# Kernel tuning notes

Measured on AMD Instinct MI355X. Metric: run time of the kernel, lower is better.

The kernel has to match this reference:

```python
import jax, jax.numpy as jnp
import numpy as np

MARGIN = 1.0  # from init_kwargs
B, H, W, P = 64, 512, 640, 100000


def setup_inputs() -> dict:
    key = jax.random.key(0)
    k0, k1, k2, k3, k4, k5 = jax.random.split(key, 6)
    return {
        "inp": jax.random.normal(k0, (B, 1, H, W), dtype=jnp.float32),
        "x_A": jax.random.randint(k1, (B, P), 0, W, dtype=jnp.int32),
        "y_A": jax.random.randint(k2, (B, P), 0, H, dtype=jnp.int32),
        "x_B": jax.random.randint(k3, (B, P), 0, W, dtype=jnp.int32),
        "y_B": jax.random.randint(k4, (B, P), 0, H, dtype=jnp.int32),
        "ordinal": jax.random.randint(k5, (B, P), 0, 3, dtype=jnp.int32),
    }


def reference(inp, x_A, y_A, x_B, y_B, ordinal):
    # inp: [B,1,H,W]; point coords: [B,P]; ordinal in {0,1,2} -> gt in {-1,0,1}
    depth = inp[:, 0]                                   # [B,H,W]
    bidx = jnp.arange(depth.shape[0])[:, None]          # [B,1]
    z_A = depth[bidx, y_A, x_A]                         # [B,P] gather
    z_B = depth[bidx, y_B, x_B]                         # [B,P] gather
    gt = (ordinal - 1).astype(depth.dtype)              # {-1,0,1}
    mask = jnp.abs(gt)
    zd = z_A - z_B
    m = jnp.asarray(MARGIN, depth.dtype)
    # ordered pairs: log(1+exp(-min(gt*zd, m))); equal pairs: max(zd^2, m^2)
    loss = mask * jnp.log(1.0 + jnp.exp(-jnp.minimum(gt * zd, m))) \
         + (1.0 - mask) * jnp.maximum(zd * zd, m * m)
    n_point_total = depth.shape[0] * x_A.shape[1]
    return jnp.sum(loss) / n_point_total
```

## Files before the change

### kernel.cpp

```cpp
#include <hip/hip_runtime.h>


constexpr int B = 64;
constexpr int H = 512;
constexpr int W = 640;
constexpr int P = 100000;
constexpr int N4B = P / 4;
constexpr int IPB = 512;
constexpr int CHUNKS = (N4B + IPB - 1) / IPB;
constexpr int NBLK = B * CHUNKS;
constexpr float INV_N = 1.0f / (float)(B * P);
constexpr float MARGIN = 1.0f;

typedef int vint4 __attribute__((ext_vector_type(4)));

__device__ __forceinline__ float loss_from(float za, float zb, int od) {
    float zd = za - zb;
    float gt = (float)(od - 1);
    float mask = fabsf(gt);
    float t = fminf(gt * zd, MARGIN);
    float l_rank = __logf(1.0f + __expf(-t));
    float l_eq = fmaxf(zd * zd, MARGIN * MARGIN);
    return mask * l_rank + (1.0f - mask) * l_eq;
}

__global__ __launch_bounds__(256) void rdc_kernel(
        const float* __restrict__ depth,
        const vint4* __restrict__ xA, const vint4* __restrict__ yA,
        const vint4* __restrict__ xB, const vint4* __restrict__ yB,
        const vint4* __restrict__ ord,
        float* __restrict__ partials) {
    __shared__ float zbuf[4][16][64];

    int j = blockIdx.x;
    int x = j & 7;
    int g = j >> 3;
    int b = ((g / CHUNKS) << 3) + x;
    int c = g % CHUNKS;
    int e0 = c * IPB + threadIdx.x;
    int e1 = e0 + 256;

    float s1 = (e1 < N4B) ? 1.0f : 0.0f;
    int i0 = b * N4B + e0;
    int i1 = b * N4B + (e1 < N4B ? e1 : e0);

    const float* d = depth + (size_t)b * (H * W);
    int lane = threadIdx.x & 63;
    int wid  = threadIdx.x >> 6;

    vint4 xa0 = __builtin_nontemporal_load(&xA[i0]);
    vint4 ya0 = __builtin_nontemporal_load(&yA[i0]);
    vint4 xb0 = __builtin_nontemporal_load(&xB[i0]);
    vint4 yb0 = __builtin_nontemporal_load(&yB[i0]);
    vint4 od0 = __builtin_nontemporal_load(&ord[i0]);
    vint4 xa1 = __builtin_nontemporal_load(&xA[i1]);
    vint4 ya1 = __builtin_nontemporal_load(&yA[i1]);
    vint4 xb1 = __builtin_nontemporal_load(&xB[i1]);
    vint4 yb1 = __builtin_nontemporal_load(&yB[i1]);
    vint4 od1 = __builtin_nontemporal_load(&ord[i1]);

    int off[16];
    off[0]  = ya0.x * W + xa0.x;  off[1]  = yb0.x * W + xb0.x;
    off[2]  = ya0.y * W + xa0.y;  off[3]  = yb0.y * W + xb0.y;
    off[4]  = ya0.z * W + xa0.z;  off[5]  = yb0.z * W + xb0.z;
    off[6]  = ya0.w * W + xa0.w;  off[7]  = yb0.w * W + xb0.w;
    off[8]  = ya1.x * W + xa1.x;  off[9]  = yb1.x * W + xb1.x;
    off[10] = ya1.y * W + xa1.y;  off[11] = yb1.y * W + xb1.y;
    off[12] = ya1.z * W + xa1.z;  off[13] = yb1.z * W + xb1.z;
    off[14] = ya1.w * W + xa1.w;  off[15] = yb1.w * W + xb1.w;

    #pragma unroll
    for (int k = 0; k < 16; ++k) {
        __builtin_amdgcn_global_load_lds(
            (const __attribute__((address_space(1))) void*)(d + off[k]),
            (__attribute__((address_space(3))) void*)&zbuf[wid][k][0],
            4, 0, 0);
    }
    __syncthreads();

    float z[16];
    #pragma unroll
    for (int k = 0; k < 16; ++k)
        z[k] = zbuf[wid][k][lane];

    float acc = 0.0f;
    acc += loss_from(z[0],  z[1],  od0.x);
    acc += loss_from(z[2],  z[3],  od0.y);
    acc += loss_from(z[4],  z[5],  od0.z);
    acc += loss_from(z[6],  z[7],  od0.w);
    float acc1 = 0.0f;
    acc1 += loss_from(z[8],  z[9],  od1.x);
    acc1 += loss_from(z[10], z[11], od1.y);
    acc1 += loss_from(z[12], z[13], od1.z);
    acc1 += loss_from(z[14], z[15], od1.w);
    acc += s1 * acc1;

    #pragma unroll
    for (int off2 = 32; off2 > 0; off2 >>= 1)
        acc += __shfl_down(acc, off2, 64);

    __shared__ float wsum[4];
    if (lane == 0) wsum[wid] = acc;
    __syncthreads();
    if (wid == 0 && lane == 0)
        partials[j] = wsum[0] + wsum[1] + wsum[2] + wsum[3];
}

__global__ __launch_bounds__(256) void rdc_finalize(
        const float* __restrict__ partials, float* __restrict__ out, int n) {
    float acc = 0.0f;
    for (int k = threadIdx.x; k < n; k += 256)
        acc += partials[k];
    #pragma unroll
    for (int off = 32; off > 0; off >>= 1)
        acc += __shfl_down(acc, off, 64);
    __shared__ float wsum[4];
    int lane = threadIdx.x & 63;
    int wid  = threadIdx.x >> 6;
    if (lane == 0) wsum[wid] = acc;
    __syncthreads();
    if (wid == 0 && lane == 0)
        out[0] = (wsum[0] + wsum[1] + wsum[2] + wsum[3]) * INV_N;
}

extern "C" void kernel_launch(void* const* d_in, const int* in_sizes, int n_in,
                              void* d_out, int out_size, void* d_ws, size_t ws_size,
                              hipStream_t stream) {
    const float* depth = (const float*)d_in[0];
    const vint4* xA = (const vint4*)d_in[1];
    const vint4* yA = (const vint4*)d_in[2];
    const vint4* xB = (const vint4*)d_in[3];
    const vint4* yB = (const vint4*)d_in[4];
    const vint4* ord = (const vint4*)d_in[5];
    float* out = (float*)d_out;

    float* partials = (float*)d_ws;
    rdc_kernel<<<NBLK, 256, 0, stream>>>(depth, xA, yA, xB, yB, ord, partials);
    rdc_finalize<<<1, 256, 0, stream>>>(partials, out, NBLK);
}
```

Baseline: 242.5 us.

## Replace random depth gathers with tiled LDS sweep over each image

Each block now owns one chunk of a batch's point pairs (8 chunks per image) and streams the whole depth image through double-buffered LDS tiles of 16K floats. Each thread keeps 56 flat pixel keys in registers and picks up values whenever a key falls in the current tile, so scattered global gathers become coalesced streaming reads. Ordinal values are packed into 2 bits to save registers. The cost is that every chunk re-reads the full image (8x per image, about 670MB in total) plus a 56-way compare loop over 20 tiles, with heavy register pressure.

```diff
diff --git a/kernel.cpp b/kernel.cpp
--- a/kernel.cpp
+++ b/kernel.cpp
@@ -5,10 +5,16 @@
 constexpr int H = 512;
 constexpr int W = 640;
 constexpr int P = 100000;
+constexpr int HWSZ = H * W;
 constexpr int N4B = P / 4;
-constexpr int IPB = 512;
-constexpr int CHUNKS = (N4B + IPB - 1) / IPB;
-constexpr int NBLK = B * CHUNKS;
+constexpr int NCHUNK = 8;
+constexpr int C4 = N4B / NCHUNK;
+constexpr int THREADS = 512;
+constexpr int SLOTS = 7;
+constexpr int NG = SLOTS * 8;
+constexpr int TE = 16384;
+constexpr int T = HWSZ / TE;
+constexpr int NBLK = B * NCHUNK;
 constexpr float INV_N = 1.0f / (float)(B * P);
 constexpr float MARGIN = 1.0f;
 
@@ -24,86 +30,110 @@
     return mask * l_rank + (1.0f - mask) * l_eq;
 }
 
-__global__ __launch_bounds__(256) void rdc_kernel(
+__device__ __forceinline__ void stage_tile(const float* __restrict__ src,
+                                           float* dst, int wid, int lane) {
+    #pragma unroll
+    for (int l = 0; l < 8; ++l) {
+        int cb = (wid * 8 + l) * 256;
+        __builtin_amdgcn_global_load_lds(
+            (const __attribute__((address_space(1))) void*)(src + cb + lane * 4),
+            (__attribute__((address_space(3))) void*)(dst + cb),
+            16, 0, 0);
+    }
+}
+
+__global__ __launch_bounds__(THREADS) void rdc_sweep(
         const float* __restrict__ depth,
         const vint4* __restrict__ xA, const vint4* __restrict__ yA,
         const vint4* __restrict__ xB, const vint4* __restrict__ yB,
         const vint4* __restrict__ ord,
         float* __restrict__ partials) {
-    __shared__ float zbuf[4][16][64];
+    __shared__ float tiles[2][TE];
+    __shared__ float wsum[8];
 
-    int j = blockIdx.x;
-    int x = j & 7;
-    int g = j >> 3;
-    int b = ((g / CHUNKS) << 3) + x;
-    int c = g % CHUNKS;
-    int e0 = c * IPB + threadIdx.x;
-    int e1 = e0 + 256;
+    const int j = blockIdx.x;
+    const int x = j & 7;
+    const int g = j >> 3;
+    const int chunk = g & 7;
+    const int b = ((g >> 3) << 3) + x;
 
-    float s1 = (e1 < N4B) ? 1.0f : 0.0f;
-    int i0 = b * N4B + e0;
-    int i1 = b * N4B + (e1 < N4B ? e1 : e0);
+    const int tid = threadIdx.x;
+    const int lane = tid & 63;
+    const int wid = tid >> 6;
 
-    const float* d = depth + (size_t)b * (H * W);
-    int lane = threadIdx.x & 63;
-    int wid  = threadIdx.x >> 6;
+    const float* dimg = depth + (size_t)b * HWSZ;
 
-    vint4 xa0 = __builtin_nontemporal_load(&xA[i0]);
-    vint4 ya0 = __builtin_nontemporal_load(&yA[i0]);
-    vint4 xb0 = __builtin_nontemporal_load(&xB[i0]);
-    vint4 yb0 = __builtin_nontemporal_load(&yB[i0]);
-    vint4 od0 = __builtin_nontemporal_load(&ord[i0]);
-    vint4 xa1 = __builtin_nontemporal_load(&xA[i1]);
-    vint4 ya1 = __builtin_nontemporal_load(&yA[i1]);
-    vint4 xb1 = __builtin_nontemporal_load(&xB[i1]);
-    vint4 yb1 = __builtin_nontemporal_load(&yB[i1]);
-    vint4 od1 = __builtin_nontemporal_load(&ord[i1]);
+    stage_tile(dimg, &tiles[0][0], wid, lane);
 
-    int off[16];
-    off[0]  = ya0.x * W + xa0.x;  off[1]  = yb0.x * W + xb0.x;
-    off[2]  = ya0.y * W + xa0.y;  off[3]  = yb0.y * W + xb0.y;
-    off[4]  = ya0.z * W + xa0.z;  off[5]  = yb0.z * W + xb0.z;
-    off[6]  = ya0.w * W + xa0.w;  off[7]  = yb0.w * W + xb0.w;
-    off[8]  = ya1.x * W + xa1.x;  off[9]  = yb1.x * W + xb1.x;
-    off[10] = ya1.y * W + xa1.y;  off[11] = yb1.y * W + xb1.y;
-    off[12] = ya1.z * W + xa1.z;  off[13] = yb1.z * W + xb1.z;
-    off[14] = ya1.w * W + xa1.w;  off[15] = yb1.w * W + xb1.w;
+    const int base4 = b * N4B + chunk * C4;
+    int key[NG];
+    int pack[SLOTS];
+    #pragma unroll
+    for (int i = 0; i < SLOTS; ++i) {
+        int c = i * THREADS + tid;
+        if (c > C4 - 1) c = C4 - 1;
+        int idx = base4 + c;
+        vint4 xa = __builtin_nontemporal_load(&xA[idx]);
+        vint4 ya = __builtin_nontemporal_load(&yA[idx]);
+        vint4 xb = __builtin_nontemporal_load(&xB[idx]);
+        vint4 yb = __builtin_nontemporal_load(&yB[idx]);
+        vint4 od = __builtin_nontemporal_load(&ord[idx]);
+        key[i*8+0] = ya.x * W + xa.x;  key[i*8+1] = yb.x * W + xb.x;
+        key[i*8+2] = ya.y * W + xa.y;  key[i*8+3] = yb.y * W + xb.y;
+        key[i*8+4] = ya.z * W + xa.z;  key[i*8+5] = yb.z * W + xb.z;
+        key[i*8+6] = ya.w * W + xa.w;  key[i*8+7] = yb.w * W + xb.w;
+        pack[i] = (od.x & 3) | ((od.y & 3) << 2) | ((od.z & 3) << 4)
+                | ((od.w & 3) << 6);
+    }
 
+    float z[NG];
     #pragma unroll
-    for (int k = 0; k < 16; ++k) {
-        __builtin_amdgcn_global_load_lds(
-            (const __attribute__((address_space(1))) void*)(d + off[k]),
-            (__attribute__((address_space(3))) void*)&zbuf[wid][k][0],
-            4, 0, 0);
+    for (int k = 0; k < NG; ++k) z[k] = 0.0f;
+
+    #pragma unroll 1
+    for (int t = 0; t < T; ++t) {
+        __syncthreads();
+        if (t + 1 < T)
+            stage_tile(dimg + (t + 1) * TE, &tiles[(t + 1) & 1][0], wid, lane);
+
+        const float* tb = &tiles[t & 1][0];
+        const int t14 = t << 14;
+        #pragma unroll
+        for (int k = 0; k < NG; ++k) {
+            unsigned rel = (unsigned)(key[k] - t14);
+            if (rel < (unsigned)TE)
+                z[k] = tb[rel];
+        }
     }
-    __syncthreads();
-
-    float z[16];
-    #pragma unroll
-    for (int k = 0; k < 16; ++k)
-        z[k] = zbuf[wid][k][lane];
 
     float acc = 0.0f;
-    acc += loss_from(z[0],  z[1],  od0.x);
-    acc += loss_from(z[2],  z[3],  od0.y);
-    acc += loss_from(z[4],  z[5],  od0.z);
-    acc += loss_from(z[6],  z[7],  od0.w);
-    float acc1 = 0.0f;
-    acc1 += loss_from(z[8],  z[9],  od1.x);
-    acc1 += loss_from(z[10], z[11], od1.y);
-    acc1 += loss_from(z[12], z[13], od1.z);
-    acc1 += loss_from(z[14], z[15], od1.w);
-    acc += s1 * acc1;
+    #pragma unroll
+    for (int i = 0; i < SLOTS; ++i) {
+        float li = 0.0f;
+        #pragma unroll
+        for (int q = 0; q < 4; ++q) {
+            int od = (pack[i] >> (2 * q)) & 3;
+            li += loss_from(z[i*8 + 2*q], z[i*8 + 2*q + 1], od);
+        }
+        if (i == SLOTS - 1) {
+            float w6 = (tid < C4 - (SLOTS - 1) * THREADS) ? 1.0f : 0.0f;
+            li *= w6;
+        }
+        acc += li;
+    }
 
     #pragma unroll
     for (int off2 = 32; off2 > 0; off2 >>= 1)
         acc += __shfl_down(acc, off2, 64);
-
-    __shared__ float wsum[4];
     if (lane == 0) wsum[wid] = acc;
     __syncthreads();
-    if (wid == 0 && lane == 0)
-        partials[j] = wsum[0] + wsum[1] + wsum[2] + wsum[3];
+    if (wid == 0) {
+        float v = (lane < 8) ? wsum[lane] : 0.0f;
+        #pragma unroll
+        for (int off2 = 4; off2 > 0; off2 >>= 1)
+            v += __shfl_down(v, off2, 64);
+        if (lane == 0) partials[j] = v;
+    }
 }
 
 __global__ __launch_bounds__(256) void rdc_finalize(
@@ -135,6 +165,6 @@
     float* out = (float*)d_out;
 
     float* partials = (float*)d_ws;
-    rdc_kernel<<<NBLK, 256, 0, stream>>>(depth, xA, yA, xB, yB, ord, partials);
+    rdc_sweep<<<NBLK, THREADS, 0, stream>>>(depth, xA, yA, xB, yB, ord, partials);
     rdc_finalize<<<1, 256, 0, stream>>>(partials, out, NBLK);
 }
```

New measurement: 313.0 us. +29.1%, slower.
